# Kernel tuning notes

Hardware: AMD Instinct MI355X
Metric: run time of the kernel (lower is better)

The kernel has to match this reference:

```python
import jax, jax.numpy as jnp
import numpy as np

B_, H_, W_, C_ = 8, 56, 56, 96
D_ = int(C_ * 2.0)          # d_inner = 192
N_ = 16                     # d_state
K_ = 4                      # scan directions
R_ = (C_ + 15) // 16        # dt_rank 'auto' = 6
MLP_H = 4 * C_
EPS = 1e-5


def setup_inputs() -> dict:
    key = jax.random.key(0)
    ks = jax.random.split(key, 16)
    s = 0.02
    rn = lambda k, sh, sc=1.0: jax.random.normal(k, sh, dtype=jnp.float32) * sc
    return dict(
        x=rn(ks[0], (B_, H_, W_, C_)),
        ln1_w=jnp.ones((C_,), jnp.float32), ln1_b=jnp.zeros((C_,), jnp.float32),
        in_proj_w=rn(ks[1], (2 * D_, C_), s),
        conv_w=rn(ks[2], (D_, 1, 3, 3), s), conv_b=jnp.zeros((D_,), jnp.float32),
        x_proj_w=rn(ks[3], (K_, R_ + 2 * N_, D_), s),
        dt_proj_w=rn(ks[4], (K_, D_, R_), s),
        dt_proj_b=rn(ks[5], (K_, D_), 0.1),
        A_logs=jax.random.uniform(ks[6], (K_ * D_, N_), jnp.float32, 0.0, 3.0),
        Ds=jnp.ones((K_ * D_,), jnp.float32),
        out_norm_w=jnp.ones((D_,), jnp.float32), out_norm_b=jnp.zeros((D_,), jnp.float32),
        out_proj_w=rn(ks[7], (C_, D_), s),
        ln2_w=jnp.ones((C_,), jnp.float32), ln2_b=jnp.zeros((C_,), jnp.float32),
        fc1_w=rn(ks[8], (MLP_H, C_), s), fc1_b=jnp.zeros((MLP_H,), jnp.float32),
        fc2_w=rn(ks[9], (C_, MLP_H), s), fc2_b=jnp.zeros((C_,), jnp.float32),
    )


def layer_norm(x, w, b):
    m = x.mean(-1, keepdims=True)
    v = ((x - m) ** 2).mean(-1, keepdims=True)
    return (x - m) / jnp.sqrt(v + EPS) * w + b


def ss2d(x, in_proj_w, conv_w, conv_b, x_proj_w, dt_proj_w, dt_proj_b,
         A_logs, Ds, out_norm_w, out_norm_b, out_proj_w):
    Bn, Hh, Ww, C = x.shape
    L = Hh * Ww
    xz = x @ in_proj_w.T                       # (B,H,W,2D)
    xc, z = jnp.split(xz, 2, axis=-1)
    xc = xc.transpose(0, 3, 1, 2)              # (B,D,H,W)
    xc = jax.lax.conv_general_dilated(xc, conv_w, (1, 1), 'SAME',
                                      feature_group_count=D_)
    xc = jax.nn.silu(xc + conv_b[None, :, None, None])
    # cross-scan: 4 traversal orders, each (B,D,L)
    x0 = xc.reshape(Bn, D_, L)
    x1 = xc.transpose(0, 1, 3, 2).reshape(Bn, D_, L)
    xs = jnp.stack([x0, x1, x0[..., ::-1], x1[..., ::-1]], axis=1)  # (B,K,D,L)
    xdbl = jnp.einsum('bkdl,kcd->bkcl', xs, x_proj_w)
    dts, Bs, Cs = jnp.split(xdbl, [R_, R_ + N_], axis=2)            # (B,K,R,L),(B,K,N,L)x2
    dts = jnp.einsum('bkrl,kdr->bkdl', dts, dt_proj_w)
    dts = jax.nn.softplus(dts + dt_proj_b[None, :, :, None])        # (B,K,D,L)
    A = -jnp.exp(A_logs).reshape(K_, D_, N_)                        # (K,D,N)

    def step(h, inp):
        xt, dtt, Bt, Ct = inp                  # (B,K,D),(B,K,D),(B,K,N),(B,K,N)
        h = h * jnp.exp(dtt[..., None] * A) + (dtt * xt)[..., None] * Bt[:, :, None, :]
        return h, jnp.einsum('bkdn,bkn->bkd', h, Ct)

    inps = (xs.transpose(3, 0, 1, 2), dts.transpose(3, 0, 1, 2),
            Bs.transpose(3, 0, 1, 2), Cs.transpose(3, 0, 1, 2))
    h0 = jnp.zeros((Bn, K_, D_, N_), jnp.float32)
    _, ys = jax.lax.scan(step, h0, inps)       # (L,B,K,D)
    ys = ys.transpose(1, 2, 3, 0)              # (B,K,D,L)
    ys = ys + Ds.reshape(K_, D_)[None, :, :, None] * xs
    # cross-merge: undo flips and transposed order
    y = ys[:, 0] + ys[:, 2, :, ::-1]
    y = y + (ys[:, 1] + ys[:, 3, :, ::-1]).reshape(Bn, D_, Ww, Hh) \
            .transpose(0, 1, 3, 2).reshape(Bn, D_, L)
    y = y.transpose(0, 2, 1).reshape(Bn, Hh, Ww, D_)
    y = layer_norm(y, out_norm_w, out_norm_b)
    y = y * jax.nn.silu(z)
    return y @ out_proj_w.T


def reference(x, ln1_w, ln1_b, in_proj_w, conv_w, conv_b, x_proj_w, dt_proj_w,
              dt_proj_b, A_logs, Ds, out_norm_w, out_norm_b, out_proj_w,
              ln2_w, ln2_b, fc1_w, fc1_b, fc2_w, fc2_b):
    # norm -> SS2D -> residual
    x = x + ss2d(layer_norm(x, ln1_w, ln1_b), in_proj_w, conv_w, conv_b,
                 x_proj_w, dt_proj_w, dt_proj_b, A_logs, Ds,
                 out_norm_w, out_norm_b, out_proj_w)
    # norm -> MLP -> residual
    h = layer_norm(x, ln2_w, ln2_b)
    h = jax.nn.gelu(h @ fc1_w.T + fc1_b) @ fc2_w.T + fc2_b
    return x + h
```

## Files before the change

kernel.cpp:

```cpp
#include <hip/hip_runtime.h>
#include <hip/hip_bf16.h>

typedef __hip_bfloat16 bf16;
typedef short bf16x8 __attribute__((ext_vector_type(8)));
typedef float f32x4 __attribute__((ext_vector_type(4)));

#define BBATCH 8
#define HHH 56
#define WWW 56
#define CCH 96
#define DIN 192
#define NST 16
#define KDIR 4
#define RDT 6
#define LLEN 3136
#define BLTOT 25088
#define SSEG 112
#define SEGL 28
#define PJC 38
#define PJW 152
#define PJS 40
#define PJS1 24
#define MLPH 384

#if defined(__has_builtin)
#if __has_builtin(__builtin_amdgcn_exp2f)
#define EXP2F(x) __builtin_amdgcn_exp2f(x)
#endif
#if __has_builtin(__builtin_amdgcn_logf)
#define LOG2F_(x) __builtin_amdgcn_logf(x)
#endif
#endif
#ifndef EXP2F
#define EXP2F(x) __expf((x) * 0.69314718056f)
#endif
#ifndef LOG2F_
#define LOG2F_(x) (__logf(x) * 1.44269504f)
#endif
#define LOG2E 1.44269504f

__device__ __forceinline__ float2 pk_mul(float2 a, float2 b) {
    float2 d;
    asm("v_pk_mul_f32 %0, %1, %2" : "=v"(d) : "v"(a), "v"(b));
    return d;
}
__device__ __forceinline__ float2 pk_fma(float2 a, float2 b, float2 c) {
    float2 d;
    asm("v_pk_fma_f32 %0, %1, %2, %3" : "=v"(d) : "v"(a), "v"(b), "v"(c));
    return d;
}

__device__ __forceinline__ float b2f(bf16 v) { return __bfloat162float(v); }
__device__ __forceinline__ bf16  f2b(float v) { return __float2bfloat16(v); }
__device__ __forceinline__ unsigned short f2bu(float f) {
    union { bf16 h; unsigned short u; } c; c.h = __float2bfloat16(f); return c.u;
}
__device__ __forceinline__ float bu2f(unsigned short u) {
    union { unsigned short u; bf16 h; } c; c.u = u; return __bfloat162float(c.h);
}
__device__ __forceinline__ float sigm(float x) { return 1.f / (1.f + __expf(-x)); }
__device__ __forceinline__ float softplusf(float x) {
    float t = EXP2F(-fabsf(x) * LOG2E);
    return fmaxf(x, 0.f) + 0.69314718f * LOG2F_(1.f + t);
}
__device__ __forceinline__ float geluf(float v) {
    float u = 0.7978845608028654f * (v + 0.044715f * v * v * v);
    float ey = __expf(2.f * u);
    float th = 1.f - 2.f / (ey + 1.f);
    return 0.5f * v * (1.f + th);
}

__device__ __forceinline__ int pos_map(int k, int l) {
    if (k & 2) l = LLEN - 1 - l;
    if (k & 1) { int q = l / WWW; int r = l - q * WWW; return r * WWW + q; }
    return l;
}

__global__ __launch_bounds__(256) void k0_pre(
    const float* __restrict__ Alog, float* __restrict__ a2g) {
    int i = blockIdx.x * 256 + threadIdx.x;
    a2g[i] = -__expf(Alog[i]) * LOG2E;
}

__global__ __launch_bounds__(256) void ln_rows(
    const float* __restrict__ xin, const float* __restrict__ w,
    const float* __restrict__ b, unsigned short* __restrict__ xn) {
    int row = blockIdx.x * 4 + (threadIdx.x >> 6);
    int lane = threadIdx.x & 63;
    const float* xr = xin + (size_t)row * 96;
    float2 v = make_float2(0.f, 0.f);
    if (lane < 48) v = *(const float2*)&xr[lane * 2];
    float s = v.x + v.y, s2 = v.x * v.x + v.y * v.y;
    for (int o = 32; o; o >>= 1) {
        s += __shfl_down(s, o);
        s2 += __shfl_down(s2, o);
    }
    s = __shfl(s, 0); s2 = __shfl(s2, 0);
    float m = s * (1.f / 96.f);
    float var = s2 * (1.f / 96.f) - m * m;
    float rs = rsqrtf(var + 1e-5f);
    if (lane < 48) {
        float o0 = (v.x - m) * rs * w[lane * 2] + b[lane * 2];
        float o1 = (v.y - m) * rs * w[lane * 2 + 1] + b[lane * 2 + 1];
        ushort2 u; u.x = f2bu(o0); u.y = f2bu(o1);
        *(ushort2*)&xn[(size_t)row * 96 + lane * 2] = u;
    }
}

template<int N, int K, int EPI>
__global__ __launch_bounds__(256) void gemm_mfma(
    const unsigned short* __restrict__ X, const float* __restrict__ W,
    const float* __restrict__ bias, const float* __restrict__ res,
    void* __restrict__ out0v, void* __restrict__ out1v) {
    __shared__ unsigned short a_sh[128 * 40];
    __shared__ unsigned short b_sh[64 * 40];
    const int t = threadIdx.x;
    const int P0 = blockIdx.x * 128;
    const int N0 = blockIdx.y * 64;
    const int w = t >> 6, lane = t & 63, q = lane >> 4, nl = lane & 15;
    f32x4 acc[2][4];
#pragma unroll
    for (int i = 0; i < 2; ++i)
#pragma unroll
        for (int j = 0; j < 4; ++j)
            acc[i][j] = (f32x4){0.f, 0.f, 0.f, 0.f};
    for (int k0 = 0; k0 < K; k0 += 32) {
        __syncthreads();
#pragma unroll
        for (int it = 0; it < 2; ++it) {
            int idx = t + it * 256;
            int pr = idx >> 2, kq = idx & 3;
            uint4 v = *(const uint4*)&X[(size_t)(P0 + pr) * K + k0 + kq * 8];
            *(uint4*)&a_sh[pr * 40 + kq * 8] = v;
        }
#pragma unroll
        for (int it = 0; it < 2; ++it) {
            int idx = t + it * 256;
            int nr = idx >> 3, kq = idx & 7;
            int ng = N0 + nr; if (ng > N - 1) ng = N - 1;
            float4 v = *(const float4*)&W[(size_t)ng * K + k0 + kq * 4];
            ushort4 u;
            u.x = f2bu(v.x); u.y = f2bu(v.y); u.z = f2bu(v.z); u.w = f2bu(v.w);
            *(ushort4*)&b_sh[nr * 40 + kq * 4] = u;
        }
        __syncthreads();
        bf16x8 af[2], bfr[4];
#pragma unroll
        for (int mf = 0; mf < 2; ++mf)
            af[mf] = *(const bf16x8*)&a_sh[(w * 32 + mf * 16 + nl) * 40 + q * 8];
#pragma unroll
        for (int nf = 0; nf < 4; ++nf)
            bfr[nf] = *(const bf16x8*)&b_sh[(nf * 16 + nl) * 40 + q * 8];
#pragma unroll
        for (int mf = 0; mf < 2; ++mf)
#pragma unroll
            for (int nf = 0; nf < 4; ++nf)
                acc[mf][nf] = __builtin_amdgcn_mfma_f32_16x16x32_bf16(
                    af[mf], bfr[nf], acc[mf][nf], 0, 0, 0);
    }
#pragma unroll
    for (int mf = 0; mf < 2; ++mf) {
#pragma unroll
        for (int nf = 0; nf < 4; ++nf) {
#pragma unroll
            for (int r = 0; r < 4; ++r) {
                float v = acc[mf][nf][r];
                size_t pos = (size_t)P0 + w * 32 + mf * 16 + q * 4 + r;
                int n = N0 + nf * 16 + nl;
                if constexpr (EPI == 0) {
                    unsigned short* xc = (unsigned short*)out0v;
                    unsigned short* zz = (unsigned short*)out1v;
                    if (n < 192) xc[pos * 192 + n] = f2bu(v);
                    else         zz[pos * 192 + (n - 192)] = f2bu(v);
                } else if constexpr (EPI == 1) {
                    if (n < 152) ((float*)out0v)[pos * 152 + n] = v;
                } else if constexpr (EPI == 2) {
                    if (n < 96) ((float*)out0v)[pos * 96 + n] = res[pos * 96 + n] + v;
                } else if constexpr (EPI == 3) {
                    ((unsigned short*)out0v)[pos * 384 + n] = f2bu(geluf(v + bias[n]));
                } else {
                    if (n < 96) ((float*)out0v)[pos * 96 + n] =
                        res[pos * 96 + n] + bias[n] + v;
                }
            }
        }
    }
}

__global__ __launch_bounds__(256) void k2_conv(
    const unsigned short* __restrict__ xcpre, const float* __restrict__ cw,
    const float* __restrict__ cb, unsigned short* __restrict__ xconv) {
    int idx = blockIdx.x * 256 + threadIdx.x;
    int dd = idx % 48;
    int P = idx / 48;
    int d0 = dd * 4;
    int b = P / LLEN, l = P - b * LLEN;
    int h = l / WWW, w = l - h * WWW;
    float acc0 = cb[d0], acc1 = cb[d0 + 1], acc2 = cb[d0 + 2], acc3 = cb[d0 + 3];
#pragma unroll
    for (int i = 0; i < 3; ++i) {
        int hh = h + i - 1;
        if (hh < 0 || hh >= HHH) continue;
#pragma unroll
        for (int j = 0; j < 3; ++j) {
            int ww = w + j - 1;
            if (ww < 0 || ww >= WWW) continue;
            ushort4 xv = *(const ushort4*)&xcpre[
                ((size_t)(b * LLEN + hh * WWW + ww)) * DIN + d0];
            acc0 = fmaf(bu2f(xv.x), cw[(d0 + 0) * 9 + i * 3 + j], acc0);
            acc1 = fmaf(bu2f(xv.y), cw[(d0 + 1) * 9 + i * 3 + j], acc1);
            acc2 = fmaf(bu2f(xv.z), cw[(d0 + 2) * 9 + i * 3 + j], acc2);
            acc3 = fmaf(bu2f(xv.w), cw[(d0 + 3) * 9 + i * 3 + j], acc3);
        }
    }
    acc0 = acc0 * sigm(acc0); acc1 = acc1 * sigm(acc1);
    acc2 = acc2 * sigm(acc2); acc3 = acc3 * sigm(acc3);
    ushort4 o;
    o.x = f2bu(acc0); o.y = f2bu(acc1); o.z = f2bu(acc2); o.w = f2bu(acc3);
    *(ushort4*)&xconv[(size_t)P * DIN + d0] = o;
}

__global__ __launch_bounds__(192) void k4_scan1(
    const bf16* __restrict__ xconv, const float* __restrict__ proj,
    const float* __restrict__ dtw, const float* __restrict__ dtb,
    const float* __restrict__ a2g, float* __restrict__ hloc,
    float* __restrict__ tsum) {
    __shared__ float pl[SEGL * PJS1];
    __shared__ int posl[SEGL];
    const int bid = blockIdx.x;
    const int s = bid % SSEG;
    const int bk = bid / SSEG;
    const int k = bk & 3, b = bk >> 2;
    const int d = threadIdx.x;
    const int l0 = s * SEGL;
    for (int q = d; q < SEGL * 22; q += 192) {
        int st = q / 22, c = q - st * 22;
        int p = pos_map(k, l0 + st);
        int ofs = (c < 6) ? c : c + 2;
        pl[st * PJS1 + ofs] = proj[(size_t)(b * LLEN + p) * PJW + k * PJC + c];
    }
    if (d < SEGL) posl[d] = pos_map(k, l0 + d) * DIN;
    float w6[RDT];
#pragma unroll
    for (int r = 0; r < RDT; ++r) w6[r] = dtw[(k * DIN + d) * RDT + r];
    const float bias = dtb[k * DIN + d];
    float2 a2[8];
#pragma unroll
    for (int j = 0; j < 8; ++j)
        a2[j] = *(const float2*)&a2g[(k * DIN + d) * NST + 2 * j];
    float2 h2[8];
#pragma unroll
    for (int j = 0; j < 8; ++j) h2[j] = make_float2(0.f, 0.f);
    float T = 0.f;
    __syncthreads();
    const bf16* xg = xconv + (size_t)b * LLEN * DIN + d;
    for (int bt = 0; bt < 4; ++bt) {
        int off7[7]; float xv7[7];
#pragma unroll
        for (int i = 0; i < 7; ++i) off7[i] = posl[bt * 7 + i];
#pragma unroll
        for (int i = 0; i < 7; ++i) xv7[i] = b2f(xg[off7[i]]);
#pragma unroll
        for (int i = 0; i < 7; ++i) {
            const float* rowf = &pl[(bt * 7 + i) * PJS1];
            float4 g0 = *(const float4*)(rowf);
            float2 g1 = *(const float2*)(rowf + 4);
            float dtv = bias;
            dtv = fmaf(g0.x, w6[0], dtv); dtv = fmaf(g0.y, w6[1], dtv);
            dtv = fmaf(g0.z, w6[2], dtv); dtv = fmaf(g0.w, w6[3], dtv);
            dtv = fmaf(g1.x, w6[4], dtv); dtv = fmaf(g1.y, w6[5], dtv);
            dtv = softplusf(dtv);
            T += dtv;
            float2 dt2 = make_float2(dtv, dtv);
            float2 u2 = make_float2(dtv * xv7[i], dtv * xv7[i]);
#pragma unroll
            for (int g = 0; g < 4; ++g) {
                float4 Bv = *(const float4*)(rowf + 8 + 4 * g);
                float2 Blo = make_float2(Bv.x, Bv.y);
                float2 Bhi = make_float2(Bv.z, Bv.w);
                float2 alo = pk_mul(dt2, a2[2 * g]);
                float2 ahi = pk_mul(dt2, a2[2 * g + 1]);
                float2 elo, ehi;
                elo.x = EXP2F(alo.x); elo.y = EXP2F(alo.y);
                ehi.x = EXP2F(ahi.x); ehi.y = EXP2F(ahi.y);
                h2[2 * g]     = pk_fma(h2[2 * g],     elo, pk_mul(u2, Blo));
                h2[2 * g + 1] = pk_fma(h2[2 * g + 1], ehi, pk_mul(u2, Bhi));
            }
        }
    }
    size_t base = ((size_t)bid * DIN + d) * NST;
#pragma unroll
    for (int j = 0; j < 8; ++j) *(float2*)&hloc[base + 2 * j] = h2[j];
    tsum[bid * DIN + d] = T;
}

__global__ __launch_bounds__(256) void k5_carry(
    const float* hloc, const float* __restrict__ tsum,
    const float* __restrict__ a2g, float* hin) {
    int g = blockIdx.x * 256 + threadIdx.x;
    int n = g & 15;
    int dk = g >> 4;
    int d = dk % DIN;
    int bk = dk / DIN;
    int k = bk & 3;
    float a2 = a2g[(k * DIN + d) * NST + n];
    float Hc = 0.f;
    for (int s = 0; s < SSEG; ++s) {
        int bid = bk * SSEG + s;
        size_t idx = ((size_t)bid * DIN + d) * NST + n;
        float hl = hloc[idx];
        float Tv = tsum[bid * DIN + d];
        hin[idx] = Hc;
        Hc = fmaf(EXP2F(a2 * Tv), Hc, hl);
    }
}

__global__ __launch_bounds__(192) void k6_scan2(
    const bf16* __restrict__ xconv, const float* __restrict__ proj,
    const float* __restrict__ dtw, const float* __restrict__ dtb,
    const float* __restrict__ a2g, const float* __restrict__ Dsp,
    const float* __restrict__ hin, bf16* __restrict__ ysm) {
    __shared__ float pl[SEGL * PJS];
    __shared__ int posl[SEGL];
    const int bid = blockIdx.x;
    const int s = bid % SSEG;
    const int bk = bid / SSEG;
    const int k = bk & 3, b = bk >> 2;
    const int d = threadIdx.x;
    const int l0 = s * SEGL;
    for (int q = d; q < SEGL * PJC; q += 192) {
        int st = q / PJC, c = q - st * PJC;
        int p = pos_map(k, l0 + st);
        int ofs = (c < 6) ? c : c + 2;
        pl[st * PJS + ofs] = proj[(size_t)(b * LLEN + p) * PJW + k * PJC + c];
    }
    if (d < SEGL) posl[d] = pos_map(k, l0 + d) * DIN;
    float w6[RDT];
#pragma unroll
    for (int r = 0; r < RDT; ++r) w6[r] = dtw[(k * DIN + d) * RDT + r];
    const float bias = dtb[k * DIN + d];
    const float dsv = Dsp[k * DIN + d];
    float2 a2[8];
#pragma unroll
    for (int j = 0; j < 8; ++j)
        a2[j] = *(const float2*)&a2g[(k * DIN + d) * NST + 2 * j];
    float2 h2[8];
    size_t hbase = ((size_t)bid * DIN + d) * NST;
#pragma unroll
    for (int j = 0; j < 8; ++j) h2[j] = *(const float2*)&hin[hbase + 2 * j];
    __syncthreads();
    const bf16* xg = xconv + (size_t)b * LLEN * DIN + d;
    bf16* ysg = ysm + ((size_t)bk * LLEN) * DIN + d;
    for (int bt = 0; bt < 4; ++bt) {
        int off7[7]; float xv7[7];
#pragma unroll
        for (int i = 0; i < 7; ++i) off7[i] = posl[bt * 7 + i];
#pragma unroll
        for (int i = 0; i < 7; ++i) xv7[i] = b2f(xg[off7[i]]);
#pragma unroll
        for (int i = 0; i < 7; ++i) {
            const float* rowf = &pl[(bt * 7 + i) * PJS];
            float4 g0 = *(const float4*)(rowf);
            float2 g1 = *(const float2*)(rowf + 4);
            float dtv = bias;
            dtv = fmaf(g0.x, w6[0], dtv); dtv = fmaf(g0.y, w6[1], dtv);
            dtv = fmaf(g0.z, w6[2], dtv); dtv = fmaf(g0.w, w6[3], dtv);
            dtv = fmaf(g1.x, w6[4], dtv); dtv = fmaf(g1.y, w6[5], dtv);
            dtv = softplusf(dtv);
            float2 dt2 = make_float2(dtv, dtv);
            float2 u2 = make_float2(dtv * xv7[i], dtv * xv7[i]);
            float2 yac0 = make_float2(0.f, 0.f), yac1 = make_float2(0.f, 0.f);
#pragma unroll
            for (int g = 0; g < 4; ++g) {
                float4 Bv = *(const float4*)(rowf + 8 + 4 * g);
                float4 Cv = *(const float4*)(rowf + 24 + 4 * g);
                float2 Blo = make_float2(Bv.x, Bv.y);
                float2 Bhi = make_float2(Bv.z, Bv.w);
                float2 Clo = make_float2(Cv.x, Cv.y);
                float2 Chi = make_float2(Cv.z, Cv.w);
                float2 alo = pk_mul(dt2, a2[2 * g]);
                float2 ahi = pk_mul(dt2, a2[2 * g + 1]);
                float2 elo, ehi;
                elo.x = EXP2F(alo.x); elo.y = EXP2F(alo.y);
                ehi.x = EXP2F(ahi.x); ehi.y = EXP2F(ahi.y);
                h2[2 * g]     = pk_fma(h2[2 * g],     elo, pk_mul(u2, Blo));
                h2[2 * g + 1] = pk_fma(h2[2 * g + 1], ehi, pk_mul(u2, Bhi));
                yac0 = pk_fma(h2[2 * g],     Clo, yac0);
                yac1 = pk_fma(h2[2 * g + 1], Chi, yac1);
            }
            float y = (yac0.x + yac0.y) + (yac1.x + yac1.y);
            ysg[off7[i]] = f2b(fmaf(dsv, xv7[i], y));
        }
    }
}

__global__ __launch_bounds__(256) void k65_merge(
    const bf16* __restrict__ ysm, const bf16* __restrict__ z,
    const float* __restrict__ onw, const float* __restrict__ onb,
    bf16* __restrict__ ymod) {
    __shared__ float rb[16 * DIN];
    __shared__ float ps[256], pq[256];
    __shared__ float mrow[16], srow[16];
    const int t = threadIdx.x;
    const int P0 = blockIdx.x * 16;
    for (int q = t; q < 16 * DIN; q += 256) {
        int pos = q / DIN, c = q - pos * DIN;
        int P = P0 + pos;
        int b = P / LLEN, l = P - b * LLEN;
        size_t base = ((size_t)(b * KDIR) * LLEN + l) * DIN + c;
        size_t pstr = (size_t)LLEN * DIN;
        float v = b2f(ysm[base]) + b2f(ysm[base + pstr]) +
                  b2f(ysm[base + 2 * pstr]) + b2f(ysm[base + 3 * pstr]);
        rb[q] = v;
    }
    __syncthreads();
    {
        int pos = t >> 4, part = t & 15;
        float s = 0.f, s2 = 0.f;
        for (int i = 0; i < 12; ++i) {
            float v = rb[pos * DIN + part * 12 + i];
            s += v; s2 += v * v;
        }
        ps[pos * 16 + part] = s; pq[pos * 16 + part] = s2;
    }
    __syncthreads();
    if (t < 16) {
        float s = 0.f, s2 = 0.f;
        for (int i = 0; i < 16; ++i) { s += ps[t * 16 + i]; s2 += pq[t * 16 + i]; }
        float m = s * (1.f / DIN);
        float v = s2 * (1.f / DIN) - m * m;
        mrow[t] = m; srow[t] = rsqrtf(v + 1e-5f);
    }
    __syncthreads();
    for (int q = t; q < 16 * DIN; q += 256) {
        int pos = q / DIN, c = q - pos * DIN;
        int P = P0 + pos;
        float v = (rb[q] - mrow[pos]) * srow[pos] * onw[c] + onb[c];
        float zv = b2f(z[(size_t)P * DIN + c]);
        v *= zv * sigm(zv);
        ymod[(size_t)P * DIN + c] = f2b(v);
    }
}

extern "C" void kernel_launch(void* const* d_in, const int* in_sizes, int n_in,
                              void* d_out, int out_size, void* d_ws, size_t ws_size,
                              hipStream_t stream) {
    const float* x      = (const float*)d_in[0];
    const float* ln1w   = (const float*)d_in[1];
    const float* ln1b   = (const float*)d_in[2];
    const float* inpW   = (const float*)d_in[3];
    const float* convW  = (const float*)d_in[4];
    const float* convB  = (const float*)d_in[5];
    const float* xprojW = (const float*)d_in[6];
    const float* dtW    = (const float*)d_in[7];
    const float* dtB    = (const float*)d_in[8];
    const float* Alog   = (const float*)d_in[9];
    const float* Dsp    = (const float*)d_in[10];
    const float* onw    = (const float*)d_in[11];
    const float* onb    = (const float*)d_in[12];
    const float* outW   = (const float*)d_in[13];
    const float* ln2w   = (const float*)d_in[14];
    const float* ln2b   = (const float*)d_in[15];
    const float* fc1W   = (const float*)d_in[16];
    const float* fc1b   = (const float*)d_in[17];
    const float* fc2W   = (const float*)d_in[18];
    const float* fc2b   = (const float*)d_in[19];
    float* out = (float*)d_out;

    char* ws = (char*)d_ws;
    unsigned short* z_us    = (unsigned short*)(ws + 0);
    bf16*  z_bf             = (bf16*)z_us;
    bf16*  xconv_bf         = (bf16*)(ws + 9633792);
    float* proj_f           = (float*)(ws + 19267584);
    bf16*  ymod_bf          = (bf16*)(ws + 19267584);
    unsigned short* xn_us   = (unsigned short*)(ws + 34521088);
    float* tsum_f           = (float*)(ws + 34521088);
    unsigned short* xcpre_us= (unsigned short*)(ws + 39337984);
    float* hloc_f           = (float*)(ws + 39337984);
    float* hin_f            = hloc_f;
    float* y1_f             = (float*)(ws + 39337984);
    unsigned short* y1n_us  = (unsigned short*)(ws + 48971776);
    bf16*  ysm_bf           = (bf16*)(ws + 83378176);
    unsigned short* hmlp_us = (unsigned short*)(ws + 83378176);
    float* a2g_f            = (float*)(ws + 121913344);

    k0_pre<<<48, 256, 0, stream>>>(Alog, a2g_f);
    ln_rows<<<6272, 256, 0, stream>>>(x, ln1w, ln1b, xn_us);
    gemm_mfma<384, 96, 0><<<dim3(196, 6), 256, 0, stream>>>(
        xn_us, inpW, nullptr, nullptr, xcpre_us, z_us);
    k2_conv<<<4704, 256, 0, stream>>>(xcpre_us, convW, convB,
                                      (unsigned short*)xconv_bf);
    gemm_mfma<152, 192, 1><<<dim3(196, 3), 256, 0, stream>>>(
        (const unsigned short*)xconv_bf, xprojW, nullptr, nullptr, proj_f, nullptr);
    k4_scan1<<<3584, 192, 0, stream>>>(xconv_bf, proj_f, dtW, dtB, a2g_f,
                                       hloc_f, tsum_f);
    k5_carry<<<384, 256, 0, stream>>>(hloc_f, tsum_f, a2g_f, hin_f);
    k6_scan2<<<3584, 192, 0, stream>>>(xconv_bf, proj_f, dtW, dtB, a2g_f, Dsp,
                                       hin_f, ysm_bf);
    k65_merge<<<1568, 256, 0, stream>>>(ysm_bf, z_bf, onw, onb, ymod_bf);
    gemm_mfma<96, 192, 2><<<dim3(196, 2), 256, 0, stream>>>(
        (const unsigned short*)ymod_bf, outW, nullptr, x, y1_f, nullptr);
    ln_rows<<<6272, 256, 0, stream>>>(y1_f, ln2w, ln2b, y1n_us);
    gemm_mfma<384, 96, 3><<<dim3(196, 6), 256, 0, stream>>>(
        y1n_us, fc1W, fc1b, nullptr, hmlp_us, nullptr);
    gemm_mfma<96, 384, 4><<<dim3(196, 2), 256, 0, stream>>>(
        hmlp_us, fc2W, fc2b, y1_f, out, nullptr);
}
```

Before: 379.5 us.

## Pre-convert GEMM weights to bf16 and split scan blocks into 64-channel chunks

A new kernel converts all five linear weight matrices to bf16 once per call, so the GEMM kernels load bf16 weight tiles directly instead of converting fp32 per tile. The two scan kernels now run 64-thread blocks, each covering a third of the channels for one segment, which triples the grid and lets more small blocks fit on each CU. The cost is that each of the three chunk blocks restages the projection rows into shared memory on its own, plus one extra small kernel launch.

```diff
diff --git a/kernel.cpp b/kernel.cpp
--- a/kernel.cpp
+++ b/kernel.cpp
@@ -82,6 +82,20 @@
     a2g[i] = -__expf(Alog[i]) * LOG2E;
 }
 
+__global__ __launch_bounds__(256) void k0w(
+    const float* __restrict__ w1, const float* __restrict__ w2,
+    const float* __restrict__ w3, const float* __restrict__ w4,
+    const float* __restrict__ w5, unsigned short* __restrict__ o) {
+    int i = blockIdx.x * 256 + threadIdx.x;
+    float v;
+    if (i < 36864)       v = w1[i];
+    else if (i < 66048)  v = w2[i - 36864];
+    else if (i < 84480)  v = w3[i - 66048];
+    else if (i < 121344) v = w4[i - 84480];
+    else                 v = w5[i - 121344];
+    o[i] = f2bu(v);
+}
+
 __global__ __launch_bounds__(256) void ln_rows(
     const float* __restrict__ xin, const float* __restrict__ w,
     const float* __restrict__ b, unsigned short* __restrict__ xn) {
@@ -109,7 +123,7 @@
 
 template<int N, int K, int EPI>
 __global__ __launch_bounds__(256) void gemm_mfma(
-    const unsigned short* __restrict__ X, const float* __restrict__ W,
+    const unsigned short* __restrict__ X, const unsigned short* __restrict__ Wb,
     const float* __restrict__ bias, const float* __restrict__ res,
     void* __restrict__ out0v, void* __restrict__ out1v) {
     __shared__ unsigned short a_sh[128 * 40];
@@ -133,15 +147,11 @@
             uint4 v = *(const uint4*)&X[(size_t)(P0 + pr) * K + k0 + kq * 8];
             *(uint4*)&a_sh[pr * 40 + kq * 8] = v;
         }
-#pragma unroll
-        for (int it = 0; it < 2; ++it) {
-            int idx = t + it * 256;
-            int nr = idx >> 3, kq = idx & 7;
+        {
+            int nr = t >> 2, kq = t & 3;
             int ng = N0 + nr; if (ng > N - 1) ng = N - 1;
-            float4 v = *(const float4*)&W[(size_t)ng * K + k0 + kq * 4];
-            ushort4 u;
-            u.x = f2bu(v.x); u.y = f2bu(v.y); u.z = f2bu(v.z); u.w = f2bu(v.w);
-            *(ushort4*)&b_sh[nr * 40 + kq * 4] = u;
+            uint4 v = *(const uint4*)&Wb[(size_t)ng * K + k0 + kq * 8];
+            *(uint4*)&b_sh[nr * 40 + kq * 8] = v;
         }
         __syncthreads();
         bf16x8 af[2], bfr[4];
@@ -220,26 +230,29 @@
     *(ushort4*)&xconv[(size_t)P * DIN + d0] = o;
 }
 
-__global__ __launch_bounds__(192) void k4_scan1(
+__global__ __launch_bounds__(64) void k4_scan1(
     const bf16* __restrict__ xconv, const float* __restrict__ proj,
     const float* __restrict__ dtw, const float* __restrict__ dtb,
     const float* __restrict__ a2g, float* __restrict__ hloc,
     float* __restrict__ tsum) {
     __shared__ float pl[SEGL * PJS1];
     __shared__ int posl[SEGL];
-    const int bid = blockIdx.x;
-    const int s = bid % SSEG;
-    const int bk = bid / SSEG;
+    const int bidx = blockIdx.x;
+    const int chunk = bidx % 3;
+    const int seg = bidx / 3;
+    const int s = seg % SSEG;
+    const int bk = seg / SSEG;
     const int k = bk & 3, b = bk >> 2;
-    const int d = threadIdx.x;
+    const int t = threadIdx.x;
+    const int d = chunk * 64 + t;
     const int l0 = s * SEGL;
-    for (int q = d; q < SEGL * 22; q += 192) {
+    for (int q = t; q < SEGL * 22; q += 64) {
         int st = q / 22, c = q - st * 22;
         int p = pos_map(k, l0 + st);
         int ofs = (c < 6) ? c : c + 2;
         pl[st * PJS1 + ofs] = proj[(size_t)(b * LLEN + p) * PJW + k * PJC + c];
     }
-    if (d < SEGL) posl[d] = pos_map(k, l0 + d) * DIN;
+    if (t < SEGL) posl[t] = pos_map(k, l0 + t) * DIN;
     float w6[RDT];
 #pragma unroll
     for (int r = 0; r < RDT; ++r) w6[r] = dtw[(k * DIN + d) * RDT + r];
@@ -288,10 +301,10 @@
             }
         }
     }
-    size_t base = ((size_t)bid * DIN + d) * NST;
+    size_t base = ((size_t)seg * DIN + d) * NST;
 #pragma unroll
     for (int j = 0; j < 8; ++j) *(float2*)&hloc[base + 2 * j] = h2[j];
-    tsum[bid * DIN + d] = T;
+    tsum[seg * DIN + d] = T;
 }
 
 __global__ __launch_bounds__(256) void k5_carry(
@@ -315,26 +328,29 @@
     }
 }
 
-__global__ __launch_bounds__(192) void k6_scan2(
+__global__ __launch_bounds__(64) void k6_scan2(
     const bf16* __restrict__ xconv, const float* __restrict__ proj,
     const float* __restrict__ dtw, const float* __restrict__ dtb,
     const float* __restrict__ a2g, const float* __restrict__ Dsp,
     const float* __restrict__ hin, bf16* __restrict__ ysm) {
     __shared__ float pl[SEGL * PJS];
     __shared__ int posl[SEGL];
-    const int bid = blockIdx.x;
-    const int s = bid % SSEG;
-    const int bk = bid / SSEG;
+    const int bidx = blockIdx.x;
+    const int chunk = bidx % 3;
+    const int seg = bidx / 3;
+    const int s = seg % SSEG;
+    const int bk = seg / SSEG;
     const int k = bk & 3, b = bk >> 2;
-    const int d = threadIdx.x;
+    const int t = threadIdx.x;
+    const int d = chunk * 64 + t;
     const int l0 = s * SEGL;
-    for (int q = d; q < SEGL * PJC; q += 192) {
+    for (int q = t; q < SEGL * PJC; q += 64) {
         int st = q / PJC, c = q - st * PJC;
         int p = pos_map(k, l0 + st);
         int ofs = (c < 6) ? c : c + 2;
         pl[st * PJS + ofs] = proj[(size_t)(b * LLEN + p) * PJW + k * PJC + c];
     }
-    if (d < SEGL) posl[d] = pos_map(k, l0 + d) * DIN;
+    if (t < SEGL) posl[t] = pos_map(k, l0 + t) * DIN;
     float w6[RDT];
 #pragma unroll
     for (int r = 0; r < RDT; ++r) w6[r] = dtw[(k * DIN + d) * RDT + r];
@@ -345,7 +361,7 @@
     for (int j = 0; j < 8; ++j)
         a2[j] = *(const float2*)&a2g[(k * DIN + d) * NST + 2 * j];
     float2 h2[8];
-    size_t hbase = ((size_t)bid * DIN + d) * NST;
+    size_t hbase = ((size_t)seg * DIN + d) * NST;
 #pragma unroll
     for (int j = 0; j < 8; ++j) h2[j] = *(const float2*)&hin[hbase + 2 * j];
     __syncthreads();
@@ -483,26 +499,29 @@
     bf16*  ysm_bf           = (bf16*)(ws + 83378176);
     unsigned short* hmlp_us = (unsigned short*)(ws + 83378176);
     float* a2g_f            = (float*)(ws + 121913344);
+    unsigned short* wbf_us  = (unsigned short*)(ws + 121962496);
 
     k0_pre<<<48, 256, 0, stream>>>(Alog, a2g_f);
+    k0w<<<618, 256, 0, stream>>>(inpW, xprojW, outW, fc1W, fc2W, wbf_us);
     ln_rows<<<6272, 256, 0, stream>>>(x, ln1w, ln1b, xn_us);
     gemm_mfma<384, 96, 0><<<dim3(196, 6), 256, 0, stream>>>(
-        xn_us, inpW, nullptr, nullptr, xcpre_us, z_us);
+        xn_us, wbf_us + 0, nullptr, nullptr, xcpre_us, z_us);
     k2_conv<<<4704, 256, 0, stream>>>(xcpre_us, convW, convB,
                                       (unsigned short*)xconv_bf);
     gemm_mfma<152, 192, 1><<<dim3(196, 3), 256, 0, stream>>>(
-        (const unsigned short*)xconv_bf, xprojW, nullptr, nullptr, proj_f, nullptr);
-    k4_scan1<<<3584, 192, 0, stream>>>(xconv_bf, proj_f, dtW, dtB, a2g_f,
+        (const unsigned short*)xconv_bf, wbf_us + 36864, nullptr, nullptr,
+        proj_f, nullptr);
+    k4_scan1<<<10752, 64, 0, stream>>>(xconv_bf, proj_f, dtW, dtB, a2g_f,
                                        hloc_f, tsum_f);
     k5_carry<<<384, 256, 0, stream>>>(hloc_f, tsum_f, a2g_f, hin_f);
-    k6_scan2<<<3584, 192, 0, stream>>>(xconv_bf, proj_f, dtW, dtB, a2g_f, Dsp,
+    k6_scan2<<<10752, 64, 0, stream>>>(xconv_bf, proj_f, dtW, dtB, a2g_f, Dsp,
                                        hin_f, ysm_bf);
     k65_merge<<<1568, 256, 0, stream>>>(ysm_bf, z_bf, onw, onb, ymod_bf);
     gemm_mfma<96, 192, 2><<<dim3(196, 2), 256, 0, stream>>>(
-        (const unsigned short*)ymod_bf, outW, nullptr, x, y1_f, nullptr);
+        (const unsigned short*)ymod_bf, wbf_us + 66048, nullptr, x, y1_f, nullptr);
     ln_rows<<<6272, 256, 0, stream>>>(y1_f, ln2w, ln2b, y1n_us);
     gemm_mfma<384, 96, 3><<<dim3(196, 6), 256, 0, stream>>>(
-        y1n_us, fc1W, fc1b, nullptr, hmlp_us, nullptr);
+        y1n_us, wbf_us + 84480, fc1b, nullptr, hmlp_us, nullptr);
     gemm_mfma<96, 384, 4><<<dim3(196, 2), 256, 0, stream>>>(
-        hmlp_us, fc2W, fc2b, y1_f, out, nullptr);
-}
+        hmlp_us, wbf_us + 121344, fc2b, y1_f, out, nullptr);
+}
```

Measured after the change: 378.7 us. No clear change (-0.2%).

## Fuse LayerNorm into GEMM prologue and pre-convert weights to bf16 once

Applied to the files above, without the earlier changes.

Removes the two standalone LayerNorm kernels and computes per-row mean and rstd inside the GEMM block, normalizing fp32 activations while staging them into shared memory. A new kernel converts all five GEMM weight matrices to bf16 once per call, so GEMM blocks load bf16 weights directly instead of converting fp32 on each tile. This saves two launches and the bf16 activation round trip through memory. In exchange, the fused GEMMs read fp32 activations, and each of the 6 N-tile blocks repeats the row statistics and normalization.

```diff
diff --git a/kernel.cpp b/kernel.cpp
--- a/kernel.cpp
+++ b/kernel.cpp
@@ -82,42 +82,52 @@
     a2g[i] = -__expf(Alog[i]) * LOG2E;
 }
 
-__global__ __launch_bounds__(256) void ln_rows(
-    const float* __restrict__ xin, const float* __restrict__ w,
-    const float* __restrict__ b, unsigned short* __restrict__ xn) {
-    int row = blockIdx.x * 4 + (threadIdx.x >> 6);
-    int lane = threadIdx.x & 63;
-    const float* xr = xin + (size_t)row * 96;
-    float2 v = make_float2(0.f, 0.f);
-    if (lane < 48) v = *(const float2*)&xr[lane * 2];
-    float s = v.x + v.y, s2 = v.x * v.x + v.y * v.y;
-    for (int o = 32; o; o >>= 1) {
-        s += __shfl_down(s, o);
-        s2 += __shfl_down(s2, o);
-    }
-    s = __shfl(s, 0); s2 = __shfl(s2, 0);
-    float m = s * (1.f / 96.f);
-    float var = s2 * (1.f / 96.f) - m * m;
-    float rs = rsqrtf(var + 1e-5f);
-    if (lane < 48) {
-        float o0 = (v.x - m) * rs * w[lane * 2] + b[lane * 2];
-        float o1 = (v.y - m) * rs * w[lane * 2 + 1] + b[lane * 2 + 1];
-        ushort2 u; u.x = f2bu(o0); u.y = f2bu(o1);
-        *(ushort2*)&xn[(size_t)row * 96 + lane * 2] = u;
-    }
-}
-
-template<int N, int K, int EPI>
+__global__ __launch_bounds__(256) void k0w(
+    const float* __restrict__ w1, const float* __restrict__ w2,
+    const float* __restrict__ w3, const float* __restrict__ w4,
+    const float* __restrict__ w5, unsigned short* __restrict__ o) {
+    int i = blockIdx.x * 256 + threadIdx.x;
+    float v;
+    if (i < 36864)       v = w1[i];
+    else if (i < 66048)  v = w2[i - 36864];
+    else if (i < 84480)  v = w3[i - 66048];
+    else if (i < 121344) v = w4[i - 84480];
+    else                 v = w5[i - 121344];
+    o[i] = f2bu(v);
+}
+
+template<int N, int K, int EPI, bool LNIN>
 __global__ __launch_bounds__(256) void gemm_mfma(
-    const unsigned short* __restrict__ X, const float* __restrict__ W,
+    const void* __restrict__ Xv, const unsigned short* __restrict__ Wb,
     const float* __restrict__ bias, const float* __restrict__ res,
+    const float* __restrict__ lnw, const float* __restrict__ lnb,
     void* __restrict__ out0v, void* __restrict__ out1v) {
     __shared__ unsigned short a_sh[128 * 40];
     __shared__ unsigned short b_sh[64 * 40];
+    __shared__ float mrow[128], rrow[128];
+    __shared__ float lnw_sh[96], lnb_sh[96];
     const int t = threadIdx.x;
     const int P0 = blockIdx.x * 128;
     const int N0 = blockIdx.y * 64;
     const int w = t >> 6, lane = t & 63, q = lane >> 4, nl = lane & 15;
+    if constexpr (LNIN) {
+        const float* Xf = (const float*)Xv;
+        const float* xr = Xf + (size_t)(P0 + (t >> 1)) * 96 + (t & 1) * 48;
+        float s = 0.f, s2 = 0.f;
+#pragma unroll
+        for (int i = 0; i < 12; ++i) {
+            float4 v = *(const float4*)&xr[i * 4];
+            s += v.x + v.y + v.z + v.w;
+            s2 += v.x * v.x + v.y * v.y + v.z * v.z + v.w * v.w;
+        }
+        s += __shfl_xor(s, 1); s2 += __shfl_xor(s2, 1);
+        if ((t & 1) == 0) {
+            float m = s * (1.f / 96.f);
+            float var = s2 * (1.f / 96.f) - m * m;
+            mrow[t >> 1] = m; rrow[t >> 1] = rsqrtf(var + 1e-5f);
+        }
+        if (t < 96) { lnw_sh[t] = lnw[t]; lnb_sh[t] = lnb[t]; }
+    }
     f32x4 acc[2][4];
 #pragma unroll
     for (int i = 0; i < 2; ++i)
@@ -130,18 +140,35 @@
         for (int it = 0; it < 2; ++it) {
             int idx = t + it * 256;
             int pr = idx >> 2, kq = idx & 3;
-            uint4 v = *(const uint4*)&X[(size_t)(P0 + pr) * K + k0 + kq * 8];
-            *(uint4*)&a_sh[pr * 40 + kq * 8] = v;
-        }
-#pragma unroll
-        for (int it = 0; it < 2; ++it) {
-            int idx = t + it * 256;
-            int nr = idx >> 3, kq = idx & 7;
+            if constexpr (LNIN) {
+                const float* Xf = (const float*)Xv;
+                const float* src = &Xf[(size_t)(P0 + pr) * K + k0 + kq * 8];
+                float m = mrow[pr], r = rrow[pr];
+                float4 v0 = *(const float4*)src;
+                float4 v1 = *(const float4*)(src + 4);
+                int c0 = k0 + kq * 8;
+                ushort4 u0, u1;
+                u0.x = f2bu((v0.x - m) * r * lnw_sh[c0+0] + lnb_sh[c0+0]);
+                u0.y = f2bu((v0.y - m) * r * lnw_sh[c0+1] + lnb_sh[c0+1]);
+                u0.z = f2bu((v0.z - m) * r * lnw_sh[c0+2] + lnb_sh[c0+2]);
+                u0.w = f2bu((v0.w - m) * r * lnw_sh[c0+3] + lnb_sh[c0+3]);
+                u1.x = f2bu((v1.x - m) * r * lnw_sh[c0+4] + lnb_sh[c0+4]);
+                u1.y = f2bu((v1.y - m) * r * lnw_sh[c0+5] + lnb_sh[c0+5]);
+                u1.z = f2bu((v1.z - m) * r * lnw_sh[c0+6] + lnb_sh[c0+6]);
+                u1.w = f2bu((v1.w - m) * r * lnw_sh[c0+7] + lnb_sh[c0+7]);
+                *(ushort4*)&a_sh[pr * 40 + kq * 8] = u0;
+                *(ushort4*)&a_sh[pr * 40 + kq * 8 + 4] = u1;
+            } else {
+                const unsigned short* X = (const unsigned short*)Xv;
+                uint4 v = *(const uint4*)&X[(size_t)(P0 + pr) * K + k0 + kq * 8];
+                *(uint4*)&a_sh[pr * 40 + kq * 8] = v;
+            }
+        }
+        {
+            int nr = t >> 2, kq = t & 3;
             int ng = N0 + nr; if (ng > N - 1) ng = N - 1;
-            float4 v = *(const float4*)&W[(size_t)ng * K + k0 + kq * 4];
-            ushort4 u;
-            u.x = f2bu(v.x); u.y = f2bu(v.y); u.z = f2bu(v.z); u.w = f2bu(v.w);
-            *(ushort4*)&b_sh[nr * 40 + kq * 4] = u;
+            uint4 v = *(const uint4*)&Wb[(size_t)ng * K + k0 + kq * 8];
+            *(uint4*)&b_sh[nr * 40 + kq * 8] = v;
         }
         __syncthreads();
         bf16x8 af[2], bfr[4];
@@ -473,36 +500,35 @@
     bf16*  xconv_bf         = (bf16*)(ws + 9633792);
     float* proj_f           = (float*)(ws + 19267584);
     bf16*  ymod_bf          = (bf16*)(ws + 19267584);
-    unsigned short* xn_us   = (unsigned short*)(ws + 34521088);
     float* tsum_f           = (float*)(ws + 34521088);
     unsigned short* xcpre_us= (unsigned short*)(ws + 39337984);
     float* hloc_f           = (float*)(ws + 39337984);
     float* hin_f            = hloc_f;
     float* y1_f             = (float*)(ws + 39337984);
-    unsigned short* y1n_us  = (unsigned short*)(ws + 48971776);
     bf16*  ysm_bf           = (bf16*)(ws + 83378176);
     unsigned short* hmlp_us = (unsigned short*)(ws + 83378176);
     float* a2g_f            = (float*)(ws + 121913344);
+    unsigned short* wbf_us  = (unsigned short*)(ws + 121962496);
 
     k0_pre<<<48, 256, 0, stream>>>(Alog, a2g_f);
-    ln_rows<<<6272, 256, 0, stream>>>(x, ln1w, ln1b, xn_us);
-    gemm_mfma<384, 96, 0><<<dim3(196, 6), 256, 0, stream>>>(
-        xn_us, inpW, nullptr, nullptr, xcpre_us, z_us);
+    k0w<<<618, 256, 0, stream>>>(inpW, xprojW, outW, fc1W, fc2W, wbf_us);
+    gemm_mfma<384, 96, 0, true><<<dim3(196, 6), 256, 0, stream>>>(
+        x, wbf_us + 0, nullptr, nullptr, ln1w, ln1b, xcpre_us, z_us);
     k2_conv<<<4704, 256, 0, stream>>>(xcpre_us, convW, convB,
                                       (unsigned short*)xconv_bf);
-    gemm_mfma<152, 192, 1><<<dim3(196, 3), 256, 0, stream>>>(
-        (const unsigned short*)xconv_bf, xprojW, nullptr, nullptr, proj_f, nullptr);
+    gemm_mfma<152, 192, 1, false><<<dim3(196, 3), 256, 0, stream>>>(
+        xconv_bf, wbf_us + 36864, nullptr, nullptr, nullptr, nullptr,
+        proj_f, nullptr);
     k4_scan1<<<3584, 192, 0, stream>>>(xconv_bf, proj_f, dtW, dtB, a2g_f,
                                        hloc_f, tsum_f);
     k5_carry<<<384, 256, 0, stream>>>(hloc_f, tsum_f, a2g_f, hin_f);
     k6_scan2<<<3584, 192, 0, stream>>>(xconv_bf, proj_f, dtW, dtB, a2g_f, Dsp,
                                        hin_f, ysm_bf);
     k65_merge<<<1568, 256, 0, stream>>>(ysm_bf, z_bf, onw, onb, ymod_bf);
-    gemm_mfma<96, 192, 2><<<dim3(196, 2), 256, 0, stream>>>(
-        (const unsigned short*)ymod_bf, outW, nullptr, x, y1_f, nullptr);
-    ln_rows<<<6272, 256, 0, stream>>>(y1_f, ln2w, ln2b, y1n_us);
-    gemm_mfma<384, 96, 3><<<dim3(196, 6), 256, 0, stream>>>(
-        y1n_us, fc1W, fc1b, nullptr, hmlp_us, nullptr);
-    gemm_mfma<96, 384, 4><<<dim3(196, 2), 256, 0, stream>>>(
-        hmlp_us, fc2W, fc2b, y1_f, out, nullptr);
-}
+    gemm_mfma<96, 192, 2, false><<<dim3(196, 2), 256, 0, stream>>>(
+        ymod_bf, wbf_us + 66048, nullptr, x, nullptr, nullptr, y1_f, nullptr);
+    gemm_mfma<384, 96, 3, true><<<dim3(196, 6), 256, 0, stream>>>(
+        y1_f, wbf_us + 84480, fc1b, nullptr, ln2w, ln2b, hmlp_us, nullptr);
+    gemm_mfma<96, 384, 4, false><<<dim3(196, 2), 256, 0, stream>>>(
+        hmlp_us, wbf_us + 121344, fc2b, y1_f, nullptr, nullptr, out, nullptr);
+}
```

Result: faster. 370.1 us (-2.5%).
